# Performance work log

Hardware: AMD Instinct MI355X
Metric: run time of the kernel (lower is better)

## Reference

```python
import jax, jax.numpy as jnp
import numpy as np

CARDS = [1000000, 500000, 100000, 50000, 10000, 10000, 5000, 5000, 1000, 1000,
         500, 500, 100, 100, 50, 50, 20, 20, 10, 10, 5, 5, 3, 3, 2, 2]

def _emb_dim(card):
    return int(min(32, max(4, round(1.6 * card ** 0.56))))

DIMS = [_emb_dim(c) for c in CARDS]          # per-table embedding dims (torch rule)
ROWS = [c + 1 for c in CARDS]                # +1 for UNK row at index 0 (padding_idx)
OFFS = np.concatenate([[0], np.cumsum(ROWS)[:-1]]).astype(np.int64)
TOTAL_ROWS = int(sum(ROWS))
MAX_D = 32
NUM_CONT = 64
B = 131072
CAT_DIM = int(sum(DIMS))                     # 508
FUSED_IN = CAT_DIM + 32                      # cont MLP outputs 32
LN_EPS = 1e-5


def setup_inputs() -> dict:
    key = jax.random.key(0)
    ks = jax.random.split(key, 10)
    x_cont = jax.random.normal(ks[0], (B, NUM_CONT), dtype=jnp.float32)
    # per-column indices in [0, card_i] (0 = UNK/padding)
    cols = [jax.random.randint(jax.random.fold_in(ks[1], i), (B,), 0, r, dtype=jnp.int64)
            for i, r in enumerate(ROWS)]
    x_cat = jnp.stack(cols, axis=1)  # [B, 26] int64
    # all tables stacked into one flat [TOTAL_ROWS, 32] array; table i uses cols [:DIMS[i]]
    emb_flat = jax.random.normal(ks[2], (TOTAL_ROWS, MAX_D), dtype=jnp.float32) * 0.05
    emb_flat = emb_flat.at[np.asarray(OFFS)].set(0.0)  # padding_idx=0 rows are zero
    # cont MLP: Linear(64,32) + LayerNorm(32) + SiLU
    Wc = jax.random.normal(ks[3], (NUM_CONT, 32), dtype=jnp.float32) * (1.0 / np.sqrt(NUM_CONT))
    bc = jnp.zeros((32,), jnp.float32)
    ln_g = jnp.ones((32,), jnp.float32)
    ln_b = jnp.zeros((32,), jnp.float32)
    # proj: Linear(540,64)+SiLU, Linear(64,32)+SiLU (dropout = identity in eval)
    W1 = jax.random.normal(ks[4], (FUSED_IN, 64), dtype=jnp.float32) * (1.0 / np.sqrt(FUSED_IN))
    b1 = jnp.zeros((64,), jnp.float32)
    W2 = jax.random.normal(ks[5], (64, 32), dtype=jnp.float32) * (1.0 / np.sqrt(64))
    b2 = jnp.zeros((32,), jnp.float32)
    return {"x_cont": x_cont, "x_cat": x_cat, "emb_flat": emb_flat,
            "Wc": Wc, "bc": bc, "ln_g": ln_g, "ln_b": ln_b,
            "W1": W1, "b1": b1, "W2": W2, "b2": b2}


def reference(x_cont, x_cat, emb_flat, Wc, bc, ln_g, ln_b, W1, b1, W2, b2):
    # --- multi-table embedding gather + concat (eval: dropout = identity) ---
    gidx = x_cat + jnp.asarray(OFFS)[None, :]          # [B, T] global row ids
    rows = emb_flat[gidx]                               # [B, T, 32] single fused gather
    rows = rows * (x_cat != 0).astype(rows.dtype)[..., None]  # padding_idx semantics
    cat = jnp.concatenate([rows[:, i, :d] for i, d in enumerate(DIMS)], axis=1)  # [B, 508]
    # --- cont MLP: Linear + LayerNorm + SiLU ---
    h = x_cont @ Wc + bc                                # [B, 32]
    mu = jnp.mean(h, axis=-1, keepdims=True)
    var = jnp.var(h, axis=-1, keepdims=True)
    h = (h - mu) / jnp.sqrt(var + LN_EPS) * ln_g + ln_b
    h = jax.nn.silu(h)
    # --- fuse + proj MLP ---
    fused = jnp.concatenate([h, cat], axis=1)           # [B, 540]
    z = jax.nn.silu(fused @ W1 + b1)                    # [B, 64]
    z = jax.nn.silu(z @ W2 + b2)                        # [B, 32]
    return z
```

## Files before the change

kernel.cpp:

```cpp
#include <hip/hip_runtime.h>

typedef __attribute__((ext_vector_type(8))) short bf16x8;
typedef __attribute__((ext_vector_type(4))) float f32x4;
typedef __attribute__((ext_vector_type(8))) unsigned short u16x8;

#define NT 26
#define BROWS 32
#define NKH 8
#define LDSTR 520
#define HSTR 36
#define Z1STR 68

__constant__ int c_OFFS[NT] = {
    0,1000001,1500002,1600003,1650004,1660005,1670006,1675007,1680008,1681009,
    1682010,1682511,1683012,1683113,1683214,1683265,1683316,1683337,1683358,
    1683369,1683380,1683386,1683392,1683396,1683400,1683403};
__constant__ int c_DIMS[NT] = {
    32,32,32,32,32,32,32,32,32,32,32,32,21,21,14,14,9,9,6,6,4,4,4,4,4,4};
__constant__ int c_COLF[NT] = {
    0,32,64,96,128,160,192,224,256,288,320,352,384,405,426,440,454,463,
    472,478,484,488,492,496,500,504};

__device__ __forceinline__ unsigned short f2bf(float f) {
  unsigned int u = __builtin_bit_cast(unsigned int, f);
  u += 0x7fffu + ((u >> 16) & 1u);
  return (unsigned short)(u >> 16);
}

__device__ __forceinline__ float silu_f(float x) {
  return x / (1.0f + __expf(-x));
}

__device__ __forceinline__ void load_bfw(const float* __restrict__ W1,
                                         bf16x8* bfw, int half, int kg, int bn) {
  #pragma unroll
  for (int ks = 0; ks < NKH; ++ks) {
    #pragma unroll
    for (int j = 0; j < 8; ++j) {
      const int k = 32 + (half << 8) + (ks << 5) + kg + j;
      const float v = (k < 540) ? W1[k * 64 + bn] : 0.0f;
      bfw[ks][j] = (short)f2bf(v);
    }
  }
}

__device__ __forceinline__ void gather_one(const float* __restrict__ emb,
                                           unsigned short* __restrict__ fused,
                                           int p, int idx) {
  const int i = p >> 5;
  const int r = p & 31;
  const float* src = emb + (size_t)(c_OFFS[i] + idx) * 32;
  unsigned short* dst = &fused[r * LDSTR + c_COLF[i]];
  const int d = c_DIMS[i];
  if (d == 32) {
    const float4* s4 = (const float4*)src;
    const float4 f0 = s4[0], f1 = s4[1], f2 = s4[2], f3 = s4[3];
    const float4 f4 = s4[4], f5 = s4[5], f6 = s4[6], f7 = s4[7];
    u16x8 o0, o1, o2, o3;
    o0[0]=f2bf(f0.x); o0[1]=f2bf(f0.y); o0[2]=f2bf(f0.z); o0[3]=f2bf(f0.w);
    o0[4]=f2bf(f1.x); o0[5]=f2bf(f1.y); o0[6]=f2bf(f1.z); o0[7]=f2bf(f1.w);
    o1[0]=f2bf(f2.x); o1[1]=f2bf(f2.y); o1[2]=f2bf(f2.z); o1[3]=f2bf(f2.w);
    o1[4]=f2bf(f3.x); o1[5]=f2bf(f3.y); o1[6]=f2bf(f3.z); o1[7]=f2bf(f3.w);
    o2[0]=f2bf(f4.x); o2[1]=f2bf(f4.y); o2[2]=f2bf(f4.z); o2[3]=f2bf(f4.w);
    o2[4]=f2bf(f5.x); o2[5]=f2bf(f5.y); o2[6]=f2bf(f5.z); o2[7]=f2bf(f5.w);
    o3[0]=f2bf(f6.x); o3[1]=f2bf(f6.y); o3[2]=f2bf(f6.z); o3[3]=f2bf(f6.w);
    o3[4]=f2bf(f7.x); o3[5]=f2bf(f7.y); o3[6]=f2bf(f7.z); o3[7]=f2bf(f7.w);
    u16x8* d8 = (u16x8*)dst;
    d8[0] = o0; d8[1] = o1; d8[2] = o2; d8[3] = o3;
  } else {
    #pragma unroll 4
    for (int c = 0; c < d; ++c) dst[c] = f2bf(src[c]);
  }
}

extern "C" __global__ void __launch_bounds__(256, 2)
tab_fused(const float* __restrict__ xc,
          const int* __restrict__ xcat,
          const float* __restrict__ emb,
          const float* __restrict__ Wc,
          const float* __restrict__ bc,
          const float* __restrict__ lng,
          const float* __restrict__ lnb,
          const float* __restrict__ W1,
          const float* __restrict__ b1,
          const float* __restrict__ W2,
          const float* __restrict__ b2,
          float* __restrict__ out) {
  __shared__ __attribute__((aligned(16))) float smem[(BROWS * LDSTR) / 2];
  __shared__ __attribute__((aligned(16))) float hf[BROWS * HSTR];
  unsigned short* fused = (unsigned short*)smem;
  float* z1 = smem;

  const int t  = threadIdx.x;
  const int w  = t >> 6;
  const int l  = t & 63;
  const int R0 = blockIdx.x * BROWS;

  const int bn = (w << 4) + (l & 15);
  const int kg = (l >> 4) << 3;
  bf16x8 bfw[NKH];
  load_bfw(W1, bfw, 0, kg, bn);
  if (t < BROWS) *(unsigned long long*)&fused[t * LDSTR + 508] = 0ull;

  int pidx[4];
  #pragma unroll
  for (int it = 0; it < 3; ++it) {
    const int p = t + it * 256;
    pidx[it] = xcat[(size_t)(R0 + (p & 31)) * NT + (p >> 5)];
  }
  if (t < 64) pidx[3] = xcat[(size_t)(R0 + (t & 31)) * NT + ((t + 768) >> 5)];
  #pragma unroll
  for (int it = 0; it < 3; ++it) gather_one(emb, fused, t + it * 256, pidx[it]);
  if (t < 64) gather_one(emb, fused, t + 768, pidx[3]);

  {
    const int r  = t >> 3;
    const int j0 = (t & 7) << 2;
    const float* xr = xc + (size_t)(R0 + r) * 64;
    float h0 = bc[j0], h1 = bc[j0 + 1], h2 = bc[j0 + 2], h3 = bc[j0 + 3];
    #pragma unroll 4
    for (int k4 = 0; k4 < 16; ++k4) {
      const float4 x4 = ((const float4*)xr)[k4];
      const float* wb = Wc + (k4 * 4) * 32 + j0;
      const float4 w0 = *(const float4*)(wb);
      const float4 w1 = *(const float4*)(wb + 32);
      const float4 w2 = *(const float4*)(wb + 64);
      const float4 w3 = *(const float4*)(wb + 96);
      h0 = __fmaf_rn(x4.x, w0.x, h0); h1 = __fmaf_rn(x4.x, w0.y, h1);
      h2 = __fmaf_rn(x4.x, w0.z, h2); h3 = __fmaf_rn(x4.x, w0.w, h3);
      h0 = __fmaf_rn(x4.y, w1.x, h0); h1 = __fmaf_rn(x4.y, w1.y, h1);
      h2 = __fmaf_rn(x4.y, w1.z, h2); h3 = __fmaf_rn(x4.y, w1.w, h3);
      h0 = __fmaf_rn(x4.z, w2.x, h0); h1 = __fmaf_rn(x4.z, w2.y, h1);
      h2 = __fmaf_rn(x4.z, w2.z, h2); h3 = __fmaf_rn(x4.z, w2.w, h3);
      h0 = __fmaf_rn(x4.w, w3.x, h0); h1 = __fmaf_rn(x4.w, w3.y, h1);
      h2 = __fmaf_rn(x4.w, w3.z, h2); h3 = __fmaf_rn(x4.w, w3.w, h3);
    }
    float s1 = h0 + h1 + h2 + h3;
    float s2 = h0 * h0 + h1 * h1 + h2 * h2 + h3 * h3;
    #pragma unroll
    for (int m = 1; m < 8; m <<= 1) {
      s1 += __shfl_xor(s1, m);
      s2 += __shfl_xor(s2, m);
    }
    const float mu = s1 * 0.03125f;
    const float var = s2 * 0.03125f - mu * mu;
    const float rs = rsqrtf(var + 1e-5f);
    float4 hv;
    hv.x = silu_f((h0 - mu) * rs * lng[j0]     + lnb[j0]);
    hv.y = silu_f((h1 - mu) * rs * lng[j0 + 1] + lnb[j0 + 1]);
    hv.z = silu_f((h2 - mu) * rs * lng[j0 + 2] + lnb[j0 + 2]);
    hv.w = silu_f((h3 - mu) * rs * lng[j0 + 3] + lnb[j0 + 3]);
    *(float4*)&hf[r * HSTR + j0] = hv;
  }
  __syncthreads();

  f32x4 acc[2];
  acc[0] = (f32x4){0.f, 0.f, 0.f, 0.f};
  acc[1] = (f32x4){0.f, 0.f, 0.f, 0.f};
  const unsigned short* arow0 = &fused[(l & 15) * LDSTR + kg];
  const unsigned short* arow1 = arow0 + 16 * LDSTR;
  #pragma unroll
  for (int ks = 0; ks < NKH; ++ks) {
    acc[0] = __builtin_amdgcn_mfma_f32_16x16x32_bf16(
        *(const bf16x8*)(arow0 + (ks << 5)), bfw[ks], acc[0], 0, 0, 0);
    acc[1] = __builtin_amdgcn_mfma_f32_16x16x32_bf16(
        *(const bf16x8*)(arow1 + (ks << 5)), bfw[ks], acc[1], 0, 0, 0);
  }
  load_bfw(W1, bfw, 1, kg, bn);
  #pragma unroll
  for (int ks = 0; ks < NKH; ++ks) {
    acc[0] = __builtin_amdgcn_mfma_f32_16x16x32_bf16(
        *(const bf16x8*)(arow0 + 256 + (ks << 5)), bfw[ks], acc[0], 0, 0, 0);
    acc[1] = __builtin_amdgcn_mfma_f32_16x16x32_bf16(
        *(const bf16x8*)(arow1 + 256 + (ks << 5)), bfw[ks], acc[1], 0, 0, 0);
  }
  __syncthreads();

  {
    float w1h[32];
    #pragma unroll
    for (int j = 0; j < 32; ++j) w1h[j] = W1[j * 64 + bn];
    const float b1v = b1[bn];
    const int rb = (l >> 4) << 2;
    #pragma unroll
    for (int mt = 0; mt < 2; ++mt) {
      #pragma unroll
      for (int v = 0; v < 4; ++v) {
        const int row = (mt << 4) + rb + v;
        const float* hrow = &hf[row * HSTR];
        float s = acc[mt][v] + b1v;
        #pragma unroll
        for (int j = 0; j < 32; ++j) s = __fmaf_rn(hrow[j], w1h[j], s);
        z1[row * Z1STR + bn] = silu_f(s);
      }
    }
  }
  __syncthreads();

  {
    const int r  = t >> 3;
    const int j0 = (t & 7) << 2;
    float a0 = b2[j0], a1 = b2[j0 + 1], a2 = b2[j0 + 2], a3 = b2[j0 + 3];
    const float* zr = &z1[r * Z1STR];
    #pragma unroll 8
    for (int k = 0; k < 64; ++k) {
      const float zv = zr[k];
      const float4 w2v = *(const float4*)(W2 + k * 32 + j0);
      a0 = __fmaf_rn(zv, w2v.x, a0);
      a1 = __fmaf_rn(zv, w2v.y, a1);
      a2 = __fmaf_rn(zv, w2v.z, a2);
      a3 = __fmaf_rn(zv, w2v.w, a3);
    }
    float4 o;
    o.x = silu_f(a0); o.y = silu_f(a1); o.z = silu_f(a2); o.w = silu_f(a3);
    *(float4*)(out + (size_t)(R0 + r) * 32 + j0) = o;
  }
}

extern "C" void kernel_launch(void* const* d_in, const int* in_sizes, int n_in,
                              void* d_out, int out_size, void* d_ws, size_t ws_size,
                              hipStream_t stream) {
  const float* xc   = (const float*)d_in[0];
  const int*   xcat = (const int*)  d_in[1];
  const float* emb  = (const float*)d_in[2];
  const float* Wc   = (const float*)d_in[3];
  const float* bc   = (const float*)d_in[4];
  const float* lng  = (const float*)d_in[5];
  const float* lnb  = (const float*)d_in[6];
  const float* W1   = (const float*)d_in[7];
  const float* b1   = (const float*)d_in[8];
  const float* W2   = (const float*)d_in[9];
  const float* b2   = (const float*)d_in[10];
  float* out = (float*)d_out;

  const int B = in_sizes[0] / 64;
  const int grid = B / BROWS;
  hipLaunchKernelGGL(tab_fused, dim3(grid), dim3(256), 0, stream,
                     xc, xcat, emb, Wc, bc, lng, lnb, W1, b1, W2, b2, out);
}
```

Baseline: 140.4 us.

## Prepack W1 into MFMA fragments and fold continuous branch into the MFMA GEMM

Adds a small prep kernel that converts W1 to bf16 and lays it out in per-lane MFMA fragment order in the workspace, with rows remapped to a padded column layout where each embedding table starts on a 4-aligned column. The main kernel then loads ready-made fragments with vector loads instead of doing strided scalar loads and conversions per block. The 32-wide continuous MLP output is written as bf16 into the fused LDS tile, so the separate fp32 FMA loop for those columns is dropped and the MFMA K-loop covers them (9 k-steps per half instead of 8). Gathers use packed v_cvt_pk_bf16_f32 conversions and vectorized stores for the small tables. The costs are an extra kernel launch per call, a larger LDS stride that may affect occupancy, and lower precision on the continuous branch.

```diff
diff --git a/kernel.cpp b/kernel.cpp
--- a/kernel.cpp
+++ b/kernel.cpp
@@ -2,22 +2,29 @@
 
 typedef __attribute__((ext_vector_type(8))) short bf16x8;
 typedef __attribute__((ext_vector_type(4))) float f32x4;
-typedef __attribute__((ext_vector_type(8))) unsigned short u16x8;
 
 #define NT 26
 #define BROWS 32
-#define NKH 8
-#define LDSTR 520
-#define HSTR 36
+#define NKH 9
+#define LDSTR 584
 #define Z1STR 68
-
-__constant__ int c_OFFS[NT] = {
-    0,1000001,1500002,1600003,1650004,1660005,1670006,1675007,1680008,1681009,
-    1682010,1682511,1683012,1683113,1683214,1683265,1683316,1683337,1683358,
-    1683369,1683380,1683386,1683392,1683396,1683400,1683403};
-__constant__ int c_DIMS[NT] = {
+#define WS_FRAG_DWORDS 18432
+
+__constant__ int4 c_TAB[NT] = {
+    {0,32,8,0},{1000001,64,8,0},{1500002,96,8,0},{1600003,128,8,0},
+    {1650004,160,8,0},{1660005,192,8,0},{1670006,224,8,0},{1675007,256,8,0},
+    {1680008,288,8,0},{1681009,320,8,0},{1682010,352,8,0},{1682511,384,8,0},
+    {1683012,416,6,0},{1683113,440,6,0},{1683214,464,4,0},{1683265,480,4,0},
+    {1683316,496,3,0},{1683337,508,3,0},{1683358,520,2,0},{1683369,528,2,0},
+    {1683380,536,1,0},{1683386,540,1,0},{1683392,544,1,0},{1683396,548,1,0},
+    {1683400,552,1,0},{1683403,556,1,0}};
+
+__constant__ int c_P_COLP[NT] = {
+    0,32,64,96,128,160,192,224,256,288,320,352,384,408,432,448,464,476,
+    488,496,504,508,512,516,520,524};
+__constant__ int c_P_DIMS[NT] = {
     32,32,32,32,32,32,32,32,32,32,32,32,21,21,14,14,9,9,6,6,4,4,4,4,4,4};
-__constant__ int c_COLF[NT] = {
+__constant__ int c_P_COLF[NT] = {
     0,32,64,96,128,160,192,224,256,288,320,352,384,405,426,440,454,463,
     472,478,484,488,492,496,500,504};
 
@@ -27,21 +34,45 @@
   return (unsigned short)(u >> 16);
 }
 
+__device__ __forceinline__ unsigned cvtpk(float a, float b) {
+  unsigned r;
+  asm("v_cvt_pk_bf16_f32 %0, %1, %2" : "=v"(r) : "v"(a), "v"(b));
+  return r;
+}
+
 __device__ __forceinline__ float silu_f(float x) {
   return x / (1.0f + __expf(-x));
 }
 
-__device__ __forceinline__ void load_bfw(const float* __restrict__ W1,
-                                         bf16x8* bfw, int half, int kg, int bn) {
-  #pragma unroll
-  for (int ks = 0; ks < NKH; ++ks) {
-    #pragma unroll
-    for (int j = 0; j < 8; ++j) {
-      const int k = 32 + (half << 8) + (ks << 5) + kg + j;
-      const float v = (k < 540) ? W1[k * 64 + bn] : 0.0f;
-      bfw[ks][j] = (short)f2bf(v);
-    }
-  }
+extern "C" __global__ void __launch_bounds__(256)
+prep_w1(const float* __restrict__ W1, unsigned int* __restrict__ wsf) {
+  const int g = blockIdx.x * 256 + threadIdx.x;
+  if (g >= WS_FRAG_DWORDS) return;
+  const int f  = g * 2;
+  const int j  = f & 7;
+  const int l  = (f >> 3) & 63;
+  const int w  = (f >> 9) & 3;
+  const int ks = f >> 11;
+  const int bn = (w << 4) + (l & 15);
+  const int k0 = (ks << 5) + ((l >> 4) << 3) + j;
+  float v[2];
+  #pragma unroll
+  for (int e = 0; e < 2; ++e) {
+    const int k = k0 + e;
+    float x = 0.0f;
+    if (k < 32) {
+      x = W1[k * 64 + bn];
+    } else {
+      const int c = k - 32;
+      for (int i = 0; i < NT; ++i) {
+        const int off = c - c_P_COLP[i];
+        if (off >= 0 && off < c_P_DIMS[i])
+          x = W1[(32 + c_P_COLF[i] + off) * 64 + bn];
+      }
+    }
+    v[e] = x;
+  }
+  wsf[g] = ((unsigned)f2bf(v[0])) | (((unsigned)f2bf(v[1])) << 16);
 }
 
 __device__ __forceinline__ void gather_one(const float* __restrict__ emb,
@@ -49,27 +80,32 @@
                                            int p, int idx) {
   const int i = p >> 5;
   const int r = p & 31;
-  const float* src = emb + (size_t)(c_OFFS[i] + idx) * 32;
-  unsigned short* dst = &fused[r * LDSTR + c_COLF[i]];
-  const int d = c_DIMS[i];
-  if (d == 32) {
-    const float4* s4 = (const float4*)src;
-    const float4 f0 = s4[0], f1 = s4[1], f2 = s4[2], f3 = s4[3];
-    const float4 f4 = s4[4], f5 = s4[5], f6 = s4[6], f7 = s4[7];
-    u16x8 o0, o1, o2, o3;
-    o0[0]=f2bf(f0.x); o0[1]=f2bf(f0.y); o0[2]=f2bf(f0.z); o0[3]=f2bf(f0.w);
-    o0[4]=f2bf(f1.x); o0[5]=f2bf(f1.y); o0[6]=f2bf(f1.z); o0[7]=f2bf(f1.w);
-    o1[0]=f2bf(f2.x); o1[1]=f2bf(f2.y); o1[2]=f2bf(f2.z); o1[3]=f2bf(f2.w);
-    o1[4]=f2bf(f3.x); o1[5]=f2bf(f3.y); o1[6]=f2bf(f3.z); o1[7]=f2bf(f3.w);
-    o2[0]=f2bf(f4.x); o2[1]=f2bf(f4.y); o2[2]=f2bf(f4.z); o2[3]=f2bf(f4.w);
-    o2[4]=f2bf(f5.x); o2[5]=f2bf(f5.y); o2[6]=f2bf(f5.z); o2[7]=f2bf(f5.w);
-    o3[0]=f2bf(f6.x); o3[1]=f2bf(f6.y); o3[2]=f2bf(f6.z); o3[3]=f2bf(f6.w);
-    o3[4]=f2bf(f7.x); o3[5]=f2bf(f7.y); o3[6]=f2bf(f7.z); o3[7]=f2bf(f7.w);
-    u16x8* d8 = (u16x8*)dst;
-    d8[0] = o0; d8[1] = o1; d8[2] = o2; d8[3] = o3;
+  const int4 tb = c_TAB[i];
+  const float4* src = (const float4*)(emb + (size_t)(tb.x + idx) * 32);
+  char* dstb = (char*)fused + r * (LDSTR * 2) + tb.y * 2;
+  if (tb.z == 8) {
+    const float4 f0 = src[0], f1 = src[1], f2 = src[2], f3 = src[3];
+    const float4 f4 = src[4], f5 = src[5], f6 = src[6], f7 = src[7];
+    uint4 o0, o1, o2, o3;
+    o0.x = cvtpk(f0.x, f0.y); o0.y = cvtpk(f0.z, f0.w);
+    o0.z = cvtpk(f1.x, f1.y); o0.w = cvtpk(f1.z, f1.w);
+    o1.x = cvtpk(f2.x, f2.y); o1.y = cvtpk(f2.z, f2.w);
+    o1.z = cvtpk(f3.x, f3.y); o1.w = cvtpk(f3.z, f3.w);
+    o2.x = cvtpk(f4.x, f4.y); o2.y = cvtpk(f4.z, f4.w);
+    o2.z = cvtpk(f5.x, f5.y); o2.w = cvtpk(f5.z, f5.w);
+    o3.x = cvtpk(f6.x, f6.y); o3.y = cvtpk(f6.z, f6.w);
+    o3.z = cvtpk(f7.x, f7.y); o3.w = cvtpk(f7.z, f7.w);
+    uint4* d4 = (uint4*)dstb;
+    d4[0] = o0; d4[1] = o1; d4[2] = o2; d4[3] = o3;
   } else {
-    #pragma unroll 4
-    for (int c = 0; c < d; ++c) dst[c] = f2bf(src[c]);
+    uint2* d2 = (uint2*)dstb;
+    for (int c4 = 0; c4 < tb.z; ++c4) {
+      const float4 fv = src[c4];
+      uint2 o;
+      o.x = cvtpk(fv.x, fv.y);
+      o.y = cvtpk(fv.z, fv.w);
+      d2[c4] = o;
+    }
   }
 }
 
@@ -81,13 +117,12 @@
           const float* __restrict__ bc,
           const float* __restrict__ lng,
           const float* __restrict__ lnb,
-          const float* __restrict__ W1,
+          const unsigned short* __restrict__ wsf,
           const float* __restrict__ b1,
           const float* __restrict__ W2,
           const float* __restrict__ b2,
           float* __restrict__ out) {
   __shared__ __attribute__((aligned(16))) float smem[(BROWS * LDSTR) / 2];
-  __shared__ __attribute__((aligned(16))) float hf[BROWS * HSTR];
   unsigned short* fused = (unsigned short*)smem;
   float* z1 = smem;
 
@@ -98,9 +133,15 @@
 
   const int bn = (w << 4) + (l & 15);
   const int kg = (l >> 4) << 3;
+
   bf16x8 bfw[NKH];
-  load_bfw(W1, bfw, 0, kg, bn);
-  if (t < BROWS) *(unsigned long long*)&fused[t * LDSTR + 508] = 0ull;
+  #pragma unroll
+  for (int ks = 0; ks < NKH; ++ks)
+    bfw[ks] = *(const bf16x8*)(wsf + (((ks) * 4 + w) * 64 + l) * 8);
+  if (t < 64) {
+    uint4 zz = {0u, 0u, 0u, 0u};
+    *(uint4*)((char*)fused + (t >> 1) * (LDSTR * 2) + (560 + (t & 1) * 8) * 2) = zz;
+  }
 
   int pidx[4];
   #pragma unroll
@@ -145,12 +186,14 @@
     const float mu = s1 * 0.03125f;
     const float var = s2 * 0.03125f - mu * mu;
     const float rs = rsqrtf(var + 1e-5f);
-    float4 hv;
-    hv.x = silu_f((h0 - mu) * rs * lng[j0]     + lnb[j0]);
-    hv.y = silu_f((h1 - mu) * rs * lng[j0 + 1] + lnb[j0 + 1]);
-    hv.z = silu_f((h2 - mu) * rs * lng[j0 + 2] + lnb[j0 + 2]);
-    hv.w = silu_f((h3 - mu) * rs * lng[j0 + 3] + lnb[j0 + 3]);
-    *(float4*)&hf[r * HSTR + j0] = hv;
+    const float g0 = silu_f((h0 - mu) * rs * lng[j0]     + lnb[j0]);
+    const float g1 = silu_f((h1 - mu) * rs * lng[j0 + 1] + lnb[j0 + 1]);
+    const float g2 = silu_f((h2 - mu) * rs * lng[j0 + 2] + lnb[j0 + 2]);
+    const float g3 = silu_f((h3 - mu) * rs * lng[j0 + 3] + lnb[j0 + 3]);
+    uint2 hw;
+    hw.x = cvtpk(g0, g1);
+    hw.y = cvtpk(g2, g3);
+    *(uint2*)((char*)fused + r * (LDSTR * 2) + j0 * 2) = hw;
   }
   __syncthreads();
 
@@ -166,20 +209,19 @@
     acc[1] = __builtin_amdgcn_mfma_f32_16x16x32_bf16(
         *(const bf16x8*)(arow1 + (ks << 5)), bfw[ks], acc[1], 0, 0, 0);
   }
-  load_bfw(W1, bfw, 1, kg, bn);
+  #pragma unroll
+  for (int ks = 0; ks < NKH; ++ks)
+    bfw[ks] = *(const bf16x8*)(wsf + (((NKH + ks) * 4 + w) * 64 + l) * 8);
   #pragma unroll
   for (int ks = 0; ks < NKH; ++ks) {
     acc[0] = __builtin_amdgcn_mfma_f32_16x16x32_bf16(
-        *(const bf16x8*)(arow0 + 256 + (ks << 5)), bfw[ks], acc[0], 0, 0, 0);
+        *(const bf16x8*)(arow0 + 288 + (ks << 5)), bfw[ks], acc[0], 0, 0, 0);
     acc[1] = __builtin_amdgcn_mfma_f32_16x16x32_bf16(
-        *(const bf16x8*)(arow1 + 256 + (ks << 5)), bfw[ks], acc[1], 0, 0, 0);
+        *(const bf16x8*)(arow1 + 288 + (ks << 5)), bfw[ks], acc[1], 0, 0, 0);
   }
   __syncthreads();
 
   {
-    float w1h[32];
-    #pragma unroll
-    for (int j = 0; j < 32; ++j) w1h[j] = W1[j * 64 + bn];
     const float b1v = b1[bn];
     const int rb = (l >> 4) << 2;
     #pragma unroll
@@ -187,11 +229,7 @@
       #pragma unroll
       for (int v = 0; v < 4; ++v) {
         const int row = (mt << 4) + rb + v;
-        const float* hrow = &hf[row * HSTR];
-        float s = acc[mt][v] + b1v;
-        #pragma unroll
-        for (int j = 0; j < 32; ++j) s = __fmaf_rn(hrow[j], w1h[j], s);
-        z1[row * Z1STR + bn] = silu_f(s);
+        z1[row * Z1STR + bn] = silu_f(acc[mt][v] + b1v);
       }
     }
   }
@@ -233,8 +271,13 @@
   const float* b2   = (const float*)d_in[10];
   float* out = (float*)d_out;
 
+  unsigned int* wsf = (unsigned int*)d_ws;
+  hipLaunchKernelGGL(prep_w1, dim3((WS_FRAG_DWORDS + 255) / 256), dim3(256),
+                     0, stream, W1, wsf);
+
   const int B = in_sizes[0] / 64;
   const int grid = B / BROWS;
   hipLaunchKernelGGL(tab_fused, dim3(grid), dim3(256), 0, stream,
-                     xc, xcat, emb, Wc, bc, lng, lnb, W1, b1, W2, b2, out);
-}
+                     xc, xcat, emb, Wc, bc, lng, lnb,
+                     (const unsigned short*)wsf, b1, W2, b2, out);
+}
```

Result: faster. 126.9 us (-9.6%).
